# Kernel tuning notes

Hardware: AMD Instinct MI355X
Metric: run time of the kernel (lower is better)

Reference implementation:

```python
import jax, jax.numpy as jnp
import numpy as np

N, E, F_IN, C, OUT = 50000, 800000, 256, 64, 2
NEG_SLOPE = 0.2  # PyG GATv2Conv default


def setup_inputs() -> dict:
    key = jax.random.key(0)
    ks = jax.random.split(key, 12)
    s = 0.05
    return {
        "x": jax.random.normal(ks[0], (N, F_IN), jnp.float32),
        "edge_index": jax.random.randint(ks[1], (2, E), 0, N, jnp.int64),
        "edge_attr": jax.random.uniform(ks[2], (E, 1), jnp.float32),
        # GATv2Conv params (heads=1): lin_l, lin_r (with bias), lin_edge (no bias), att, conv bias
        "Wl": jax.random.normal(ks[3], (C, F_IN), jnp.float32) * s,
        "bl": jax.random.normal(ks[4], (C,), jnp.float32) * s,
        "Wr": jax.random.normal(ks[5], (C, F_IN), jnp.float32) * s,
        "br": jax.random.normal(ks[6], (C,), jnp.float32) * s,
        "We": jax.random.normal(ks[7], (C, 1), jnp.float32) * s,
        "att": jax.random.normal(ks[8], (C,), jnp.float32) * s,
        "b_conv": jax.random.normal(ks[9], (C,), jnp.float32) * s,
        # final linear head
        "W_head": jax.random.normal(ks[10], (OUT, C), jnp.float32) * s,
        "b_head": jax.random.normal(ks[11], (OUT,), jnp.float32) * s,
    }


def reference(x, edge_index, edge_attr, Wl, bl, Wr, br, We, att, b_conv, W_head, b_head):
    n = x.shape[0]
    xl = x @ Wl.T + bl  # [N, C] source transform (values)
    xr = x @ Wr.T + br  # [N, C] destination transform
    src, dst = edge_index[0], edge_index[1]

    # add self loops; self-loop edge_attr = mean of incoming edge attrs (fill_value='mean')
    cnt = jax.ops.segment_sum(jnp.ones(src.shape, x.dtype), dst, num_segments=n)
    loop_attr = jax.ops.segment_sum(edge_attr, dst, num_segments=n) / jnp.clip(cnt, 1.0)[:, None]
    ar = jnp.arange(n, dtype=src.dtype)
    src2 = jnp.concatenate([src, ar])
    dst2 = jnp.concatenate([dst, ar])
    ea2 = jnp.concatenate([edge_attr, loop_attr], axis=0)

    # GATv2 attention: score = att . leaky_relu(xl[src] + xr[dst] + We @ ea)
    m = xl[src2] + xr[dst2] + ea2 @ We.T  # [E+N, C]
    e = jnp.sum(jax.nn.leaky_relu(m, NEG_SLOPE) * att, axis=-1)  # [E+N]

    # per-destination softmax (every node has a self loop -> no empty segments)
    emax = jax.lax.stop_gradient(jax.ops.segment_max(e, dst2, num_segments=n))
    ee = jnp.exp(e - emax[dst2])
    denom = jax.ops.segment_sum(ee, dst2, num_segments=n)
    alpha = ee / denom[dst2]  # [E+N]

    out = jax.ops.segment_sum(alpha[:, None] * xl[src2], dst2, num_segments=n) + b_conv  # [N, C]

    h = jax.nn.relu(out)                      # dropout is identity in eval mode
    pooled = jnp.mean(h, axis=0, keepdims=True)  # MeanAggregation over all nodes -> [1, C]
    logits = pooled @ W_head.T + b_head          # [1, 2]
    return jax.nn.softmax(logits, axis=-1)
```

## Files before the change

kernel.cpp:

```cpp
#include <hip/hip_runtime.h>

constexpr int NN   = 50000;
constexpr int EE   = 800000;
constexpr float NEG_SLOPE = 0.2f;
constexpr int MAXDEG = 64;

typedef __attribute__((ext_vector_type(4))) float f32x4;
typedef __attribute__((ext_vector_type(8))) short bf16x8;

constexpr size_t OFF_XLB  = 0;
constexpr size_t OFF_XRB  = OFF_XLB + (size_t)NN * 64 * 2;
constexpr size_t OFF_H    = OFF_XRB + (size_t)NN * 64 * 2;
constexpr size_t OFF_FILL = OFF_H   + (size_t)NN * 64 * 4;
constexpr size_t OFF_POOL = OFF_FILL+ (size_t)NN * 4;
constexpr size_t OFF_CSRP = OFF_POOL+ 256;
constexpr size_t ZERO_BYTES = (size_t)NN * 4 + 256;

__device__ __forceinline__ unsigned short f2bf(float f) {
    unsigned u = __float_as_uint(f);
    unsigned r = (u + 0x7FFFu + ((u >> 16) & 1u)) >> 16;
    return (unsigned short)r;
}
__device__ __forceinline__ float bf2f(unsigned s) {
    return __uint_as_float(s << 16);
}

constexpr int GEMM_BLOCKS = 391;
constexpr int SCAT_BLOCKS = 512;
constexpr int GEMM_WAVES  = GEMM_BLOCKS * 8;
constexpr int NSTRIP      = NN / 16;

__global__ __launch_bounds__(512, 2)
void fused_gemm_scatter(const float* __restrict__ x,
                        const float* __restrict__ Wl, const float* __restrict__ bl,
                        const float* __restrict__ Wr, const float* __restrict__ br,
                        unsigned short* __restrict__ xlb, unsigned short* __restrict__ xrb,
                        const int* __restrict__ ei, const float* __restrict__ ea,
                        int* __restrict__ fill, unsigned* __restrict__ csrp) {
    if (blockIdx.x >= GEMM_BLOCKS) {
        const int b = blockIdx.x - GEMM_BLOCKS;
        for (int e = b * 512 + threadIdx.x; e < EE; e += SCAT_BLOCKS * 512) {
            int src = ei[e];
            int dst = ei[EE + e];
            unsigned pk = (unsigned)src | ((unsigned)f2bf(ea[e]) << 16);
            int k = atomicAdd(&fill[dst], 1);
            if (k < MAXDEG) csrp[(size_t)dst * MAXDEG + k] = pk;
        }
        return;
    }

    extern __shared__ bf16x8 Wf[];
    const int tid  = threadIdx.x;
    const int lane = tid & 63;
    const int w    = tid >> 6;

    for (int idx = tid; idx < 4096; idx += 512) {
        int cb = idx >> 9;
        int ks = (idx >> 6) & 7;
        int l  = idx & 63;
        int r16 = l & 15, g = l >> 4;
        const float* wsrc = (cb < 4) ? (Wl + (size_t)(16 * cb + r16) * 256)
                                     : (Wr + (size_t)(16 * (cb - 4) + r16) * 256);
        int k0 = 32 * ks + 8 * g;
        float4 w0 = *reinterpret_cast<const float4*>(wsrc + k0);
        float4 w1 = *reinterpret_cast<const float4*>(wsrc + k0 + 4);
        bf16x8 pk;
        pk[0] = (short)f2bf(w0.x); pk[1] = (short)f2bf(w0.y);
        pk[2] = (short)f2bf(w0.z); pk[3] = (short)f2bf(w0.w);
        pk[4] = (short)f2bf(w1.x); pk[5] = (short)f2bf(w1.y);
        pk[6] = (short)f2bf(w1.z); pk[7] = (short)f2bf(w1.w);
        Wf[idx] = pk;
    }

    const int col15 = lane & 15;
    const int g4    = lane >> 4;
    float bias[8];
    #pragma unroll
    for (int cb = 0; cb < 8; ++cb)
        bias[cb] = (cb < 4) ? bl[16 * cb + col15] : br[16 * (cb - 4) + col15];
    __syncthreads();

    const int gw = blockIdx.x * 8 + w;
    for (int strip = gw; strip < NSTRIP; strip += GEMM_WAVES) {
        const int r0 = strip * 16;
        const float* xrow = x + (size_t)(r0 + col15) * 256 + 8 * g4;

        f32x4 acc[8];
        #pragma unroll
        for (int cb = 0; cb < 8; ++cb) acc[cb] = (f32x4){0.f, 0.f, 0.f, 0.f};

        #pragma unroll
        for (int ks = 0; ks < 8; ++ks) {
            float4 a0 = *reinterpret_cast<const float4*>(xrow + 32 * ks);
            float4 a1 = *reinterpret_cast<const float4*>(xrow + 32 * ks + 4);
            bf16x8 af;
            af[0] = (short)f2bf(a0.x); af[1] = (short)f2bf(a0.y);
            af[2] = (short)f2bf(a0.z); af[3] = (short)f2bf(a0.w);
            af[4] = (short)f2bf(a1.x); af[5] = (short)f2bf(a1.y);
            af[6] = (short)f2bf(a1.z); af[7] = (short)f2bf(a1.w);
            #pragma unroll
            for (int cb = 0; cb < 8; ++cb) {
                bf16x8 bfg = Wf[(cb * 8 + ks) * 64 + lane];
                acc[cb] = __builtin_amdgcn_mfma_f32_16x16x32_bf16(af, bfg, acc[cb], 0, 0, 0);
            }
        }

        #pragma unroll
        for (int cb = 0; cb < 8; ++cb) {
            unsigned short* dst = (cb < 4) ? xlb : xrb;
            int c0 = (cb & 3) * 16 + col15;
            #pragma unroll
            for (int r = 0; r < 4; ++r) {
                int row = r0 + 4 * g4 + r;
                dst[(size_t)row * 64 + c0] = f2bf(acc[cb][r] + bias[cb]);
            }
        }
    }
}

__global__ __launch_bounds__(256)
void attn_kernel(const unsigned short* __restrict__ xlb, const unsigned short* __restrict__ xrb,
                 const unsigned* __restrict__ csrp, const int* __restrict__ fill,
                 const float* __restrict__ We, const float* __restrict__ att,
                 const float* __restrict__ bconv, float* __restrict__ h) {
    const int v = blockIdx.x * 4 + (threadIdx.x >> 6);
    const int c = threadIdx.x & 63;

    const float wec = We[c], attc = att[c];
    const float xrc = bf2f(xrb[(size_t)v * 64 + c]);
    const float xlc = bf2f(xlb[(size_t)v * 64 + c]);
    int deg = fill[v];
    deg = __builtin_amdgcn_readfirstlane(deg);
    const int degc = (deg > MAXDEG) ? MAXDEG : deg;
    const unsigned* bucket = csrp + (size_t)v * MAXDEG;

    float dA = 0.f, dB = 0.f, aA = 0.f, aB = 0.f, asum = 0.f;

    int i = 0;
    for (; i + 8 <= degc; i += 8) {
        unsigned e0 = bucket[i],     e1 = bucket[i + 1], e2 = bucket[i + 2], e3 = bucket[i + 3];
        unsigned e4 = bucket[i + 4], e5 = bucket[i + 5], e6 = bucket[i + 6], e7 = bucket[i + 7];
        float at0 = bf2f(e0 >> 16), at1 = bf2f(e1 >> 16), at2 = bf2f(e2 >> 16), at3 = bf2f(e3 >> 16);
        float at4 = bf2f(e4 >> 16), at5 = bf2f(e5 >> 16), at6 = bf2f(e6 >> 16), at7 = bf2f(e7 >> 16);
        float x0 = bf2f(xlb[(size_t)(e0 & 0xFFFFu) * 64 + c]);
        float x1 = bf2f(xlb[(size_t)(e1 & 0xFFFFu) * 64 + c]);
        float x2 = bf2f(xlb[(size_t)(e2 & 0xFFFFu) * 64 + c]);
        float x3 = bf2f(xlb[(size_t)(e3 & 0xFFFFu) * 64 + c]);
        float x4 = bf2f(xlb[(size_t)(e4 & 0xFFFFu) * 64 + c]);
        float x5 = bf2f(xlb[(size_t)(e5 & 0xFFFFu) * 64 + c]);
        float x6 = bf2f(xlb[(size_t)(e6 & 0xFFFFu) * 64 + c]);
        float x7 = bf2f(xlb[(size_t)(e7 & 0xFFFFu) * 64 + c]);
        asum += (at0 + at1 + at2 + at3) + (at4 + at5 + at6 + at7);

        float m, s0, s1, s2, s3, s4, s5, s6, s7;
        m = fmaf(wec, at0, x0 + xrc); s0 = fmaf(NEG_SLOPE, fminf(m, 0.f), fmaxf(m, 0.f)) * attc;
        m = fmaf(wec, at1, x1 + xrc); s1 = fmaf(NEG_SLOPE, fminf(m, 0.f), fmaxf(m, 0.f)) * attc;
        m = fmaf(wec, at2, x2 + xrc); s2 = fmaf(NEG_SLOPE, fminf(m, 0.f), fmaxf(m, 0.f)) * attc;
        m = fmaf(wec, at3, x3 + xrc); s3 = fmaf(NEG_SLOPE, fminf(m, 0.f), fmaxf(m, 0.f)) * attc;
        m = fmaf(wec, at4, x4 + xrc); s4 = fmaf(NEG_SLOPE, fminf(m, 0.f), fmaxf(m, 0.f)) * attc;
        m = fmaf(wec, at5, x5 + xrc); s5 = fmaf(NEG_SLOPE, fminf(m, 0.f), fmaxf(m, 0.f)) * attc;
        m = fmaf(wec, at6, x6 + xrc); s6 = fmaf(NEG_SLOPE, fminf(m, 0.f), fmaxf(m, 0.f)) * attc;
        m = fmaf(wec, at7, x7 + xrc); s7 = fmaf(NEG_SLOPE, fminf(m, 0.f), fmaxf(m, 0.f)) * attc;

        #pragma unroll
        for (int d = 1; d < 64; d <<= 1) {
            s0 += __shfl_xor(s0, d); s1 += __shfl_xor(s1, d);
            s2 += __shfl_xor(s2, d); s3 += __shfl_xor(s3, d);
            s4 += __shfl_xor(s4, d); s5 += __shfl_xor(s5, d);
            s6 += __shfl_xor(s6, d); s7 += __shfl_xor(s7, d);
        }

        float p;
        p = __expf(s0); dA += p; aA = fmaf(p, x0, aA);
        p = __expf(s1); dB += p; aB = fmaf(p, x1, aB);
        p = __expf(s2); dA += p; aA = fmaf(p, x2, aA);
        p = __expf(s3); dB += p; aB = fmaf(p, x3, aB);
        p = __expf(s4); dA += p; aA = fmaf(p, x4, aA);
        p = __expf(s5); dB += p; aB = fmaf(p, x5, aB);
        p = __expf(s6); dA += p; aA = fmaf(p, x6, aA);
        p = __expf(s7); dB += p; aB = fmaf(p, x7, aB);
    }
    for (; i < degc; ++i) {
        unsigned e = bucket[i];
        float at = bf2f(e >> 16);
        float xx = bf2f(xlb[(size_t)(e & 0xFFFFu) * 64 + c]);
        asum += at;
        float m = fmaf(wec, at, xx + xrc);
        float s = fmaf(NEG_SLOPE, fminf(m, 0.f), fmaxf(m, 0.f)) * attc;
        #pragma unroll
        for (int d = 1; d < 64; d <<= 1) s += __shfl_xor(s, d);
        float p = __expf(s);
        dA += p; aA = fmaf(p, xx, aA);
    }

    {
        float lattr = asum / fmaxf((float)deg, 1.0f);
        float m = fmaf(wec, lattr, xlc + xrc);
        float s = fmaf(NEG_SLOPE, fminf(m, 0.f), fmaxf(m, 0.f)) * attc;
        #pragma unroll
        for (int d = 1; d < 64; d <<= 1) s += __shfl_xor(s, d);
        float p = __expf(s);
        dA += p; aA = fmaf(p, xlc, aA);
    }

    float outv = (aA + aB) / (dA + dB) + bconv[c];
    h[(size_t)v * 64 + c] = fmaxf(outv, 0.0f);
}

__global__ void pool_kernel(const float* __restrict__ h, float* __restrict__ pool) {
    __shared__ float s[256];
    const int c = threadIdx.x & 63, g = threadIdx.x >> 6;
    float acc = 0.f;
    for (int r = blockIdx.x * 4 + g; r < NN; r += gridDim.x * 4)
        acc += h[(size_t)r * 64 + c];
    s[threadIdx.x] = acc;
    __syncthreads();
    if (threadIdx.x < 64) {
        float tot = s[c] + s[64 + c] + s[128 + c] + s[192 + c];
        atomicAdd(&pool[c], tot);
    }
}

__global__ void head_kernel(const float* __restrict__ pool, const float* __restrict__ Wh,
                            const float* __restrict__ bh, float* __restrict__ out) {
    const int c = threadIdx.x;
    float p  = pool[c] * (1.0f / (float)NN);
    float a0 = p * Wh[c];
    float a1 = p * Wh[64 + c];
    #pragma unroll
    for (int d = 1; d < 64; d <<= 1) { a0 += __shfl_xor(a0, d); a1 += __shfl_xor(a1, d); }
    if (c == 0) {
        float l0 = a0 + bh[0], l1 = a1 + bh[1];
        float mx = fmaxf(l0, l1);
        float e0 = __expf(l0 - mx), e1 = __expf(l1 - mx);
        float inv = 1.0f / (e0 + e1);
        out[0] = e0 * inv;
        out[1] = e1 * inv;
    }
}

extern "C" void kernel_launch(void* const* d_in, const int* in_sizes, int n_in,
                              void* d_out, int out_size, void* d_ws, size_t ws_size,
                              hipStream_t stream) {
    const float* x    = (const float*)d_in[0];
    const int*   ei   = (const int*)  d_in[1];
    const float* ea   = (const float*)d_in[2];
    const float* Wl   = (const float*)d_in[3];
    const float* bl   = (const float*)d_in[4];
    const float* Wr   = (const float*)d_in[5];
    const float* br   = (const float*)d_in[6];
    const float* We   = (const float*)d_in[7];
    const float* att  = (const float*)d_in[8];
    const float* bcv  = (const float*)d_in[9];
    const float* Wh   = (const float*)d_in[10];
    const float* bh   = (const float*)d_in[11];
    float* out = (float*)d_out;

    char* ws = (char*)d_ws;
    unsigned short* xlb = (unsigned short*)(ws + OFF_XLB);
    unsigned short* xrb = (unsigned short*)(ws + OFF_XRB);
    float*    h    = (float*)   (ws + OFF_H);
    int*      fill = (int*)     (ws + OFF_FILL);
    float*    pool = (float*)   (ws + OFF_POOL);
    unsigned* csrp = (unsigned*)(ws + OFF_CSRP);

    hipMemsetAsync(ws + OFF_FILL, 0, ZERO_BYTES, stream);

    fused_gemm_scatter<<<GEMM_BLOCKS + SCAT_BLOCKS, 512, 4096 * sizeof(bf16x8), stream>>>(
        x, Wl, bl, Wr, br, xlb, xrb, ei, ea, fill, csrp);

    attn_kernel<<<NN / 4, 256, 0, stream>>>(xlb, xrb, csrp, fill, We, att, bcv, h);

    pool_kernel<<<128, 256, 0, stream>>>(h, pool);
    head_kernel<<<1, 64, 0, stream>>>(pool, Wh, bh, out);
}
```

Before: 239.6 us.

## Split scatter fill counters into 8 regions and stage edge buckets in LDS

```diff
diff --git a/kernel.cpp b/kernel.cpp
--- a/kernel.cpp
+++ b/kernel.cpp
@@ -3,18 +3,21 @@
 constexpr int NN   = 50000;
 constexpr int EE   = 800000;
 constexpr float NEG_SLOPE = 0.2f;
-constexpr int MAXDEG = 64;
+constexpr int NREG  = 8;
+constexpr int RCAP  = 16;
+constexpr int SLOTS = NREG * RCAP;
+constexpr int PSROWS = NN / 4;
 
 typedef __attribute__((ext_vector_type(4))) float f32x4;
 typedef __attribute__((ext_vector_type(8))) short bf16x8;
 
-constexpr size_t OFF_XLB  = 0;
-constexpr size_t OFF_XRB  = OFF_XLB + (size_t)NN * 64 * 2;
-constexpr size_t OFF_H    = OFF_XRB + (size_t)NN * 64 * 2;
-constexpr size_t OFF_FILL = OFF_H   + (size_t)NN * 64 * 4;
-constexpr size_t OFF_POOL = OFF_FILL+ (size_t)NN * 4;
-constexpr size_t OFF_CSRP = OFF_POOL+ 256;
-constexpr size_t ZERO_BYTES = (size_t)NN * 4 + 256;
+constexpr size_t OFF_XLB   = 0;
+constexpr size_t OFF_XRB   = OFF_XLB  + (size_t)NN * 64 * 2;
+constexpr size_t OFF_PSUM  = OFF_XRB  + (size_t)NN * 64 * 2;
+constexpr size_t OFF_FILL8 = OFF_PSUM + (size_t)PSROWS * 64 * 4;
+constexpr size_t OFF_POOL  = OFF_FILL8+ (size_t)NREG * NN * 4;
+constexpr size_t OFF_CSRP  = OFF_POOL + 256;
+constexpr size_t ZERO_BYTES = (size_t)NREG * NN * 4 + 256;
 
 __device__ __forceinline__ unsigned short f2bf(float f) {
     unsigned u = __float_as_uint(f);
@@ -36,15 +39,17 @@
                         const float* __restrict__ Wr, const float* __restrict__ br,
                         unsigned short* __restrict__ xlb, unsigned short* __restrict__ xrb,
                         const int* __restrict__ ei, const float* __restrict__ ea,
-                        int* __restrict__ fill, unsigned* __restrict__ csrp) {
+                        int* __restrict__ fill8, unsigned* __restrict__ csrp) {
     if (blockIdx.x >= GEMM_BLOCKS) {
-        const int b = blockIdx.x - GEMM_BLOCKS;
+        const int b   = blockIdx.x - GEMM_BLOCKS;
+        const int reg = blockIdx.x & 7;
+        int* fr = fill8 + reg * NN;
         for (int e = b * 512 + threadIdx.x; e < EE; e += SCAT_BLOCKS * 512) {
             int src = ei[e];
             int dst = ei[EE + e];
             unsigned pk = (unsigned)src | ((unsigned)f2bf(ea[e]) << 16);
-            int k = atomicAdd(&fill[dst], 1);
-            if (k < MAXDEG) csrp[(size_t)dst * MAXDEG + k] = pk;
+            int k = atomicAdd(&fr[dst], 1);
+            if (k < RCAP) csrp[(size_t)dst * SLOTS + reg * RCAP + k] = pk;
         }
         return;
     }
@@ -120,36 +125,73 @@
 
 __global__ __launch_bounds__(256)
 void attn_kernel(const unsigned short* __restrict__ xlb, const unsigned short* __restrict__ xrb,
-                 const unsigned* __restrict__ csrp, const int* __restrict__ fill,
+                 const uint2* __restrict__ csrp2, const int* __restrict__ fill8,
                  const float* __restrict__ We, const float* __restrict__ att,
-                 const float* __restrict__ bconv, float* __restrict__ h) {
-    const int v = blockIdx.x * 4 + (threadIdx.x >> 6);
-    const int c = threadIdx.x & 63;
+                 const float* __restrict__ bconv, float* __restrict__ psum) {
+    __shared__ unsigned ebuf[4][SLOTS];
+    __shared__ float sred[256];
+    const int wid = threadIdx.x >> 6;
+    const int c   = threadIdx.x & 63;
+    const int v   = blockIdx.x * 4 + wid;
 
     const float wec = We[c], attc = att[c];
     const float xrc = bf2f(xrb[(size_t)v * 64 + c]);
     const float xlc = bf2f(xlb[(size_t)v * 64 + c]);
-    int deg = fill[v];
-    deg = __builtin_amdgcn_readfirstlane(deg);
-    const int degc = (deg > MAXDEG) ? MAXDEG : deg;
-    const unsigned* bucket = csrp + (size_t)v * MAXDEG;
-
+
+    uint2 ep   = csrp2[(size_t)v * (SLOTS / 2) + c];
+    int   myr  = c >> 3;
+    int   mycnt = fill8[myr * NN + v];
+    int   mycc  = min(mycnt, RCAP);
+    int prefC = 0, degT = 0, degC = 0;
+    #pragma unroll
+    for (int r = 0; r < 8; ++r) {
+        int cr = __shfl(mycnt, r * 8);
+        int cc = min(cr, RCAP);
+        degT += cr; degC += cc;
+        if (r < myr) prefC += cc;
+    }
+    int k0 = (2 * c) & 15;
+    if (k0     < mycc) ebuf[wid][prefC + k0]     = ep.x;
+    if (k0 + 1 < mycc) ebuf[wid][prefC + k0 + 1] = ep.y;
+    __syncthreads();
+
+    const unsigned* eb = ebuf[wid];
     float dA = 0.f, dB = 0.f, aA = 0.f, aB = 0.f, asum = 0.f;
 
-    int i = 0;
-    for (; i + 8 <= degc; i += 8) {
-        unsigned e0 = bucket[i],     e1 = bucket[i + 1], e2 = bucket[i + 2], e3 = bucket[i + 3];
-        unsigned e4 = bucket[i + 4], e5 = bucket[i + 5], e6 = bucket[i + 6], e7 = bucket[i + 7];
-        float at0 = bf2f(e0 >> 16), at1 = bf2f(e1 >> 16), at2 = bf2f(e2 >> 16), at3 = bf2f(e3 >> 16);
-        float at4 = bf2f(e4 >> 16), at5 = bf2f(e5 >> 16), at6 = bf2f(e6 >> 16), at7 = bf2f(e7 >> 16);
-        float x0 = bf2f(xlb[(size_t)(e0 & 0xFFFFu) * 64 + c]);
-        float x1 = bf2f(xlb[(size_t)(e1 & 0xFFFFu) * 64 + c]);
-        float x2 = bf2f(xlb[(size_t)(e2 & 0xFFFFu) * 64 + c]);
-        float x3 = bf2f(xlb[(size_t)(e3 & 0xFFFFu) * 64 + c]);
-        float x4 = bf2f(xlb[(size_t)(e4 & 0xFFFFu) * 64 + c]);
-        float x5 = bf2f(xlb[(size_t)(e5 & 0xFFFFu) * 64 + c]);
-        float x6 = bf2f(xlb[(size_t)(e6 & 0xFFFFu) * 64 + c]);
-        float x7 = bf2f(xlb[(size_t)(e7 & 0xFFFFu) * 64 + c]);
+    const int nch = degC >> 3;
+    uint4 EA, EB, FA, FB;
+    float x0, x1, x2, x3, x4, x5, x6, x7;
+    float y0, y1, y2, y3, y4, y5, y6, y7;
+
+    if (nch > 0) {
+        EA = *reinterpret_cast<const uint4*>(&eb[0]);
+        EB = *reinterpret_cast<const uint4*>(&eb[4]);
+        x0 = bf2f(xlb[(size_t)(EA.x & 0xFFFFu) * 64 + c]);
+        x1 = bf2f(xlb[(size_t)(EA.y & 0xFFFFu) * 64 + c]);
+        x2 = bf2f(xlb[(size_t)(EA.z & 0xFFFFu) * 64 + c]);
+        x3 = bf2f(xlb[(size_t)(EA.w & 0xFFFFu) * 64 + c]);
+        x4 = bf2f(xlb[(size_t)(EB.x & 0xFFFFu) * 64 + c]);
+        x5 = bf2f(xlb[(size_t)(EB.y & 0xFFFFu) * 64 + c]);
+        x6 = bf2f(xlb[(size_t)(EB.z & 0xFFFFu) * 64 + c]);
+        x7 = bf2f(xlb[(size_t)(EB.w & 0xFFFFu) * 64 + c]);
+    }
+    for (int ch = 0; ch < nch; ++ch) {
+        if (ch + 1 < nch) {
+            FA = *reinterpret_cast<const uint4*>(&eb[(ch + 1) * 8]);
+            FB = *reinterpret_cast<const uint4*>(&eb[(ch + 1) * 8 + 4]);
+            y0 = bf2f(xlb[(size_t)(FA.x & 0xFFFFu) * 64 + c]);
+            y1 = bf2f(xlb[(size_t)(FA.y & 0xFFFFu) * 64 + c]);
+            y2 = bf2f(xlb[(size_t)(FA.z & 0xFFFFu) * 64 + c]);
+            y3 = bf2f(xlb[(size_t)(FA.w & 0xFFFFu) * 64 + c]);
+            y4 = bf2f(xlb[(size_t)(FB.x & 0xFFFFu) * 64 + c]);
+            y5 = bf2f(xlb[(size_t)(FB.y & 0xFFFFu) * 64 + c]);
+            y6 = bf2f(xlb[(size_t)(FB.z & 0xFFFFu) * 64 + c]);
+            y7 = bf2f(xlb[(size_t)(FB.w & 0xFFFFu) * 64 + c]);
+        }
+        float at0 = bf2f(EA.x >> 16), at1 = bf2f(EA.y >> 16);
+        float at2 = bf2f(EA.z >> 16), at3 = bf2f(EA.w >> 16);
+        float at4 = bf2f(EB.x >> 16), at5 = bf2f(EB.y >> 16);
+        float at6 = bf2f(EB.z >> 16), at7 = bf2f(EB.w >> 16);
         asum += (at0 + at1 + at2 + at3) + (at4 + at5 + at6 + at7);
 
         float m, s0, s1, s2, s3, s4, s5, s6, s7;
@@ -179,9 +221,13 @@
         p = __expf(s5); dB += p; aB = fmaf(p, x5, aB);
         p = __expf(s6); dA += p; aA = fmaf(p, x6, aA);
         p = __expf(s7); dB += p; aB = fmaf(p, x7, aB);
-    }
-    for (; i < degc; ++i) {
-        unsigned e = bucket[i];
+
+        EA = FA; EB = FB;
+        x0 = y0; x1 = y1; x2 = y2; x3 = y3;
+        x4 = y4; x5 = y5; x6 = y6; x7 = y7;
+    }
+    for (int j = nch * 8; j < degC; ++j) {
+        unsigned e = eb[j];
         float at = bf2f(e >> 16);
         float xx = bf2f(xlb[(size_t)(e & 0xFFFFu) * 64 + c]);
         asum += at;
@@ -194,7 +240,7 @@
     }
 
     {
-        float lattr = asum / fmaxf((float)deg, 1.0f);
+        float lattr = asum / fmaxf((float)degT, 1.0f);
         float m = fmaf(wec, lattr, xlc + xrc);
         float s = fmaf(NEG_SLOPE, fminf(m, 0.f), fmaxf(m, 0.f)) * attc;
         #pragma unroll
@@ -203,16 +249,21 @@
         dA += p; aA = fmaf(p, xlc, aA);
     }
 
-    float outv = (aA + aB) / (dA + dB) + bconv[c];
-    h[(size_t)v * 64 + c] = fmaxf(outv, 0.0f);
-}
-
-__global__ void pool_kernel(const float* __restrict__ h, float* __restrict__ pool) {
+    float outv = fmaxf((aA + aB) / (dA + dB) + bconv[c], 0.0f);
+    sred[threadIdx.x] = outv;
+    __syncthreads();
+    if (threadIdx.x < 64) {
+        psum[(size_t)blockIdx.x * 64 + c] =
+            sred[c] + sred[64 + c] + sred[128 + c] + sred[192 + c];
+    }
+}
+
+__global__ void pool_kernel(const float* __restrict__ psum, float* __restrict__ pool) {
     __shared__ float s[256];
     const int c = threadIdx.x & 63, g = threadIdx.x >> 6;
     float acc = 0.f;
-    for (int r = blockIdx.x * 4 + g; r < NN; r += gridDim.x * 4)
-        acc += h[(size_t)r * 64 + c];
+    for (int r = blockIdx.x * 4 + g; r < PSROWS; r += gridDim.x * 4)
+        acc += psum[(size_t)r * 64 + c];
     s[threadIdx.x] = acc;
     __syncthreads();
     if (threadIdx.x < 64) {
@@ -259,18 +310,19 @@
     char* ws = (char*)d_ws;
     unsigned short* xlb = (unsigned short*)(ws + OFF_XLB);
     unsigned short* xrb = (unsigned short*)(ws + OFF_XRB);
-    float*    h    = (float*)   (ws + OFF_H);
-    int*      fill = (int*)     (ws + OFF_FILL);
-    float*    pool = (float*)   (ws + OFF_POOL);
-    unsigned* csrp = (unsigned*)(ws + OFF_CSRP);
-
-    hipMemsetAsync(ws + OFF_FILL, 0, ZERO_BYTES, stream);
+    float*    psum  = (float*)   (ws + OFF_PSUM);
+    int*      fill8 = (int*)     (ws + OFF_FILL8);
+    float*    pool  = (float*)   (ws + OFF_POOL);
+    unsigned* csrp  = (unsigned*)(ws + OFF_CSRP);
+
+    hipMemsetAsync(ws + OFF_FILL8, 0, ZERO_BYTES, stream);
 
     fused_gemm_scatter<<<GEMM_BLOCKS + SCAT_BLOCKS, 512, 4096 * sizeof(bf16x8), stream>>>(
-        x, Wl, bl, Wr, br, xlb, xrb, ei, ea, fill, csrp);
-
-    attn_kernel<<<NN / 4, 256, 0, stream>>>(xlb, xrb, csrp, fill, We, att, bcv, h);
-
-    pool_kernel<<<128, 256, 0, stream>>>(h, pool);
+        x, Wl, bl, Wr, br, xlb, xrb, ei, ea, fill8, csrp);
+
+    attn_kernel<<<NN / 4, 256, 0, stream>>>(xlb, xrb, (const uint2*)csrp, fill8,
+                                            We, att, bcv, psum);
+
+    pool_kernel<<<64, 256, 0, stream>>>(psum, pool);
     head_kernel<<<1, 64, 0, stream>>>(pool, Wh, bh, out);
 }
```

Result: faster. 234.7 us (-2.1%).
